# Kernel optimization log

Hardware: AMD Instinct MI355X
Metric: run time of the kernel (lower is better)

The kernel has to match this reference:

```python
import jax, jax.numpy as jnp
import numpy as np

B, H, D, K, V, M = 64, 32, 4096, 128, 128, 4095

def setup_inputs() -> dict:
    key = jax.random.key(0)
    ks = jax.random.split(key, 7)
    return {
        "x": jax.random.normal(ks[0], (B, D), dtype=jnp.float32),
        "prev_K": jax.random.normal(ks[1], (B, M, K), dtype=jnp.float32),
        "prev_V": jax.random.normal(ks[2], (B, M, V), dtype=jnp.float32),
        "Wq": jax.random.normal(ks[3], (H, D, K), dtype=jnp.float32),
        "Wk": jax.random.normal(ks[4], (D, K), dtype=jnp.float32),
        "Wv": jax.random.normal(ks[5], (D, V), dtype=jnp.float32),
        "Wo": jax.random.normal(ks[6], (H, V, D), dtype=jnp.float32),
    }

def reference(x, prev_K, prev_V, Wq, Wk, Wv, Wo):
    # Projections
    q = jnp.einsum('bd,hdk->bhk', x, Wq)            # [b,h,k]
    k_new = jnp.einsum('bd,dk->bk', x, Wk)          # [b,k]
    v_new = jnp.einsum('bd,dv->bv', x, Wv)          # [b,v]
    Kc = jnp.concatenate([prev_K, k_new[:, None, :]], axis=1)  # [b,m+1,k]
    Vc = jnp.concatenate([prev_V, v_new[:, None, :]], axis=1)  # [b,m+1,v]
    # Shared-KV attention (MQA)
    logits = jnp.einsum('bhk,bmk->bhm', q, Kc)
    weights = jax.nn.softmax(logits, axis=-1)
    o = jnp.einsum('bhm,bmv->bhv', weights, Vc)
    y = jnp.einsum('bhv,hvd->bd', o, Wo)
    return (y, Kc, Vc)
```

## Files before the change

kernel.cpp:

```cpp
#include <hip/hip_runtime.h>
#include <stdint.h>

#define B_  64
#define H_  32
#define D_  4096
#define KD  128
#define VD  128
#define M_  4095
#define M1_ 4096
#define NCHUNK 32
#define LOG2E 1.44269504088896f

#define WS_P      0ull
#define WS_Q      4456448ull
#define WS_STATS  4718592ull
#define WS_O      4849664ull
#define WS_OPART  5111808ull

#define WAITVL(n) asm volatile("s_waitcnt vmcnt(" #n ") lgkmcnt(0)" ::: "memory")
#define WAITL()  asm volatile("s_waitcnt lgkmcnt(0)" ::: "memory")
#define BAR()    __builtin_amdgcn_s_barrier()

typedef __attribute__((address_space(3))) char lds_char;
typedef const __attribute__((address_space(1))) char glb_char;

__global__ __launch_bounds__(256) void k_proj_partial(
    const float* __restrict__ x, const float* __restrict__ Wq,
    const float* __restrict__ Wk, const float* __restrict__ Wv,
    float* __restrict__ P) {
  __shared__ float xs[64][260];
  const int dc = blockIdx.x;
  const int hx = blockIdx.y;
  const int t  = threadIdx.x;
  const float* xsrc = x + dc * 256;
  #pragma unroll
  for (int j = 0; j < 16; ++j) {
    int f = t + 256 * j;
    int row = f >> 6, c4 = f & 63;
    *(float4*)&xs[row][c4 * 4] =
        *(const float4*)(xsrc + (size_t)row * D_ + c4 * 4);
  }
  __syncthreads();
  const int bq = t >> 4;
  const int kg = t & 15;
  const int b0 = bq * 4;
  const float* W = (hx < H_) ? (Wq + (size_t)hx * D_ * KD)
                             : ((hx == H_) ? Wk : Wv);
  const float* wp = W + (size_t)(dc * 256) * KD + kg * 8;
  float acc[4][8];
  #pragma unroll
  for (int i = 0; i < 4; ++i)
    #pragma unroll
    for (int j = 0; j < 8; ++j) acc[i][j] = 0.f;
  #pragma unroll 8
  for (int d = 0; d < 256; ++d) {
    float4 w0 = *(const float4*)(wp + (size_t)d * KD);
    float4 w1 = *(const float4*)(wp + (size_t)d * KD + 4);
    float xv[4];
    #pragma unroll
    for (int i = 0; i < 4; ++i) xv[i] = xs[b0 + i][d];
    #pragma unroll
    for (int i = 0; i < 4; ++i) {
      acc[i][0] += xv[i] * w0.x; acc[i][1] += xv[i] * w0.y;
      acc[i][2] += xv[i] * w0.z; acc[i][3] += xv[i] * w0.w;
      acc[i][4] += xv[i] * w1.x; acc[i][5] += xv[i] * w1.y;
      acc[i][6] += xv[i] * w1.z; acc[i][7] += xv[i] * w1.w;
    }
  }
  #pragma unroll
  for (int i = 0; i < 4; ++i) {
    size_t base = ((size_t)(dc * 64 + b0 + i) * 34 + hx) * KD + kg * 8;
    *(float4*)&P[base]     = make_float4(acc[i][0], acc[i][1], acc[i][2], acc[i][3]);
    *(float4*)&P[base + 4] = make_float4(acc[i][4], acc[i][5], acc[i][6], acc[i][7]);
  }
}

__global__ __launch_bounds__(256) void k_proj_reduce(
    const float* __restrict__ P, float* __restrict__ q,
    float* __restrict__ Kc, float* __restrict__ Vc) {
  int i = blockIdx.x * 256 + threadIdx.x;
  int k = i & 127;
  int hx = (i >> 7) % 34;
  int b = i / (128 * 34);
  float s = 0.f;
  #pragma unroll
  for (int dc = 0; dc < 16; ++dc)
    s += P[(size_t)dc * (64 * 34 * 128) + (size_t)(b * 34 + hx) * 128 + k];
  if (hx < H_)       q[((size_t)b * H_ + hx) * KD + k] = s;
  else if (hx == H_) Kc[((size_t)b * M1_ + M_) * KD + k] = s;
  else               Vc[((size_t)b * M1_ + M_) * VD + k] = s;
}

__device__ __forceinline__ void stage_issue(
    const float* src, const float* app_row, float* lbuf, int m_lo, int t) {
  const int wb = t & ~63;
  #pragma unroll
  for (int j = 0; j < 4; ++j) {
    int f = j * 256 + t;
    int r = f >> 5, p = f & 31;
    int m = m_lo + r;
    int g4 = p ^ (r & 7);
    const float* gp = (m < M_) ? (src + (size_t)m * 128 + g4 * 4)
                               : (app_row + g4 * 4);
    __builtin_amdgcn_global_load_lds(
        (glb_char*)gp, (lds_char*)(lbuf + (size_t)(j * 256 + wb) * 4),
        16, 0, 0);
  }
}

__device__ __forceinline__ void copy_out(
    const float* lbuf, float* dst, int m_lo, int t) {
  #pragma unroll
  for (int jj = 0; jj < 4; ++jj) {
    int f = jj * 256 + t;
    int r = f >> 5, p = f & 31;
    int g4 = p ^ (r & 7);
    float4 v = *(const float4*)&lbuf[(size_t)f * 4];
    *(float4*)(dst + (size_t)(m_lo + r) * 128 + g4 * 4) = v;
  }
}

__global__ __launch_bounds__(256, 3) void k_flash(
    const float* __restrict__ prevK, const float* __restrict__ prevV,
    const float* __restrict__ q, float* __restrict__ Kc, float* __restrict__ Vc,
    float* __restrict__ o_part, float* __restrict__ stats) {
  __shared__ float buf[2][32 * 128];
  __shared__ float upool[4608];
  __shared__ float swl[4 * 64];
  const int chunk = blockIdx.x;
  const int b = blockIdx.y;
  const int t = threadIdx.x;
  const int m0 = chunk * 128;
  const int w = t >> 6, l = t & 63;

  const float* kbase = prevK + (size_t)b * M_ * KD;
  const float* vbase = prevV + (size_t)b * M_ * VD;
  const float* kapp  = Kc + ((size_t)b * M1_ + M_) * KD;
  const float* vapp  = Vc + ((size_t)b * M1_ + M_) * VD;
  float* kc = Kc + (size_t)b * M1_ * KD;
  float* vc = Vc + (size_t)b * M1_ * VD;

  float* kslice = &buf[0][0] + w * 2048;
  const int mw = m0 + w * 32;

#define KSTAGE(S)                                                             \
  {                                                                           \
    float* dst_ = kslice + ((S) & 1) * 1024;                                  \
    _Pragma("unroll")                                                         \
    for (int j = 0; j < 4; ++j) {                                             \
      int f4 = j * 64 + l;                                                    \
      int r = f4 >> 5, p = f4 & 31;                                           \
      int m = mw + (S) * 8 + r;                                               \
      int g4 = p ^ r;                                                         \
      const float* gp = (m < M_) ? (kbase + (size_t)m * 128 + g4 * 4)         \
                                 : (kapp + g4 * 4);                           \
      __builtin_amdgcn_global_load_lds(                                       \
          (glb_char*)gp, (lds_char*)(dst_ + j * 256), 16, 0, 0);              \
    }                                                                         \
  }

#define KCOPY(S)                                                              \
  {                                                                           \
    const float* s_ = kslice + ((S) & 1) * 1024;                              \
    _Pragma("unroll")                                                         \
    for (int jj = 0; jj < 4; ++jj) {                                          \
      int f4 = jj * 64 + l;                                                   \
      int r = f4 >> 5, p = f4 & 31;                                           \
      int g4 = p ^ r;                                                         \
      float4 v = *(const float4*)&s_[f4 * 4];                                 \
      *(float4*)(kc + (size_t)(mw + (S) * 8 + r) * 128 + g4 * 4) = v;         \
    }                                                                         \
  }

  const float* qsrc = q + (size_t)b * H_ * KD;
  float4 qv4[4];
  #pragma unroll
  for (int j = 0; j < 4; ++j) {
    int f = j * 256 + t;
    qv4[j] = *(const float4*)(qsrc + (size_t)(f >> 5) * KD + (f & 31) * 4);
  }
  KSTAGE(0); KSTAGE(1);
  #pragma unroll
  for (int j = 0; j < 4; ++j) {
    int f = j * 256 + t;
    int row = f >> 5, c4 = f & 31;
    *(float4*)&upool[row * 128 + ((c4 ^ ((row >> 1) & 7)) * 4)] = qv4[j];
  }

  const int rp = l & 3, hg = l >> 2, h0 = hg * 2;
  const int qsw = hg & 7;
  const int v4 = t & 31, hoct = t >> 5, h0v = hoct * 4;

  float accL0[8], accL1[8];

#define KLOG(S)                                                               \
  {                                                                           \
    const float* lb = kslice + ((S) & 1) * 1024;                              \
    float c00 = 0.f, c01 = 0.f, c10 = 0.f, c11 = 0.f;                         \
    _Pragma("unroll 8")                                                       \
    for (int k4 = 0; k4 < 32; ++k4) {                                         \
      int qp = (k4 ^ qsw) * 4;          \
      float4 qa = *(const float4*)&upool[h0 * 128 + qp];                      \
      float4 qb = *(const float4*)&upool[(h0 + 1) * 128 + qp];                \
      float4 k0v = *(const float4*)&lb[(rp * 32 + (k4 ^ rp)) * 4];            \
      float4 k1v = *(const float4*)&lb[((rp + 4) * 32 + (k4 ^ (rp + 4))) * 4];\
      c00 += qa.x*k0v.x + qa.y*k0v.y + qa.z*k0v.z + qa.w*k0v.w;               \
      c01 += qa.x*k1v.x + qa.y*k1v.y + qa.z*k1v.z + qa.w*k1v.w;               \
      c10 += qb.x*k0v.x + qb.y*k0v.y + qb.z*k0v.z + qb.w*k0v.w;               \
      c11 += qb.x*k1v.x + qb.y*k1v.y + qb.z*k1v.z + qb.w*k1v.w;               \
    }                                                                         \
    accL0[(S)*2] = c00; accL0[(S)*2+1] = c01;                                 \
    accL1[(S)*2] = c10; accL1[(S)*2+1] = c11;                                 \
  }

#define PV_TILE(S, BUFI)                                                      \
  {                                                                           \
    const float* lb = &buf[BUFI][0];                                          \
    _Pragma("unroll 4")                                                       \
    for (int mm = 0; mm < 32; ++mm) {                                         \
      int p = (v4 ^ (mm & 7)) * 4;                                            \
      float4 gv = *(const float4*)&lb[mm * 128 + p];                          \
      float4 w4 = *(const float4*)&upool[((S) * 32 + mm) * 36 + h0v];         \
      a0.x += w4.x*gv.x; a0.y += w4.x*gv.y; a0.z += w4.x*gv.z; a0.w += w4.x*gv.w; \
      a1.x += w4.y*gv.x; a1.y += w4.y*gv.y; a1.z += w4.y*gv.z; a1.w += w4.y*gv.w; \
      a2.x += w4.z*gv.x; a2.y += w4.z*gv.y; a2.z += w4.z*gv.z; a2.w += w4.z*gv.w; \
      a3.x += w4.w*gv.x; a3.y += w4.w*gv.y; a3.z += w4.w*gv.z; a3.w += w4.w*gv.w; \
    }                                                                         \
  }

  WAITL(); BAR();

  WAITVL(4);  KLOG(0); KCOPY(0); KSTAGE(2);
  WAITVL(8);  KLOG(1); KCOPY(1); KSTAGE(3);
  WAITVL(8);  KLOG(2); KCOPY(2);
  WAITVL(4);  KLOG(3); KCOPY(3);

  float mx0 = -3.402823466e38f, mx1 = -3.402823466e38f;
  #pragma unroll
  for (int j = 0; j < 8; ++j) {
    mx0 = fmaxf(mx0, accL0[j]);
    mx1 = fmaxf(mx1, accL1[j]);
  }
  mx0 = fmaxf(mx0, __shfl_xor(mx0, 1)); mx0 = fmaxf(mx0, __shfl_xor(mx0, 2));
  mx1 = fmaxf(mx1, __shfl_xor(mx1, 1)); mx1 = fmaxf(mx1, __shfl_xor(mx1, 2));
  float s0 = 0.f, s1 = 0.f;
  #pragma unroll
  for (int j = 0; j < 8; ++j) {
    float e0 = exp2f((accL0[j] - mx0) * LOG2E); accL0[j] = e0; s0 += e0;
    float e1 = exp2f((accL1[j] - mx1) * LOG2E); accL1[j] = e1; s1 += e1;
  }
  s0 += __shfl_xor(s0, 1); s0 += __shfl_xor(s0, 2);
  s1 += __shfl_xor(s1, 1); s1 += __shfl_xor(s1, 2);
  if (rp == 0)
    *(float4*)&swl[w * 64 + h0 * 2] = make_float4(mx0, s0, mx1, s1);
  WAITL(); BAR();

  stage_issue(vbase, vapp, &buf[0][0], m0, t);
  float cm0, cs0, cm1, cs1;
  {
    float4 r0 = *(const float4*)&swl[0 * 64 + h0 * 2];
    float4 r1 = *(const float4*)&swl[1 * 64 + h0 * 2];
    float4 r2 = *(const float4*)&swl[2 * 64 + h0 * 2];
    float4 r3 = *(const float4*)&swl[3 * 64 + h0 * 2];
    cm0 = fmaxf(fmaxf(r0.x, r1.x), fmaxf(r2.x, r3.x));
    cm1 = fmaxf(fmaxf(r0.z, r1.z), fmaxf(r2.z, r3.z));
    cs0 = r0.y * exp2f((r0.x - cm0) * LOG2E) + r1.y * exp2f((r1.x - cm0) * LOG2E)
        + r2.y * exp2f((r2.x - cm0) * LOG2E) + r3.y * exp2f((r3.x - cm0) * LOG2E);
    cs1 = r0.w * exp2f((r0.z - cm1) * LOG2E) + r1.w * exp2f((r1.z - cm1) * LOG2E)
        + r2.w * exp2f((r2.z - cm1) * LOG2E) + r3.w * exp2f((r3.z - cm1) * LOG2E);
    float f0 = exp2f((mx0 - cm0) * LOG2E);
    float f1 = exp2f((mx1 - cm1) * LOG2E);
    #pragma unroll
    for (int S = 0; S < 4; ++S)
      #pragma unroll
      for (int half = 0; half < 2; ++half) {
        int m = w * 32 + S * 8 + rp + 4 * half;
        upool[m * 36 + h0]     = accL0[S * 2 + half] * f0;
        upool[m * 36 + h0 + 1] = accL1[S * 2 + half] * f1;
      }
  }
  stage_issue(vbase, vapp, &buf[1][0], m0 + 32, t);
  WAITVL(4); BAR();

  float4 a0 = {0,0,0,0}, a1 = {0,0,0,0}, a2 = {0,0,0,0}, a3 = {0,0,0,0};

  PV_TILE(0, 0); copy_out(&buf[0][0], vc, m0, t);
  WAITL(); BAR();
  stage_issue(vbase, vapp, &buf[0][0], m0 + 64, t);
  WAITVL(8); BAR();
  PV_TILE(1, 1); copy_out(&buf[1][0], vc, m0 + 32, t);
  WAITL(); BAR();
  stage_issue(vbase, vapp, &buf[1][0], m0 + 96, t);
  WAITVL(8); BAR();
  PV_TILE(2, 0); copy_out(&buf[0][0], vc, m0 + 64, t);
  WAITVL(4); BAR();
  PV_TILE(3, 1); copy_out(&buf[1][0], vc, m0 + 96, t);

  size_t base = ((size_t)(chunk * B_ + b) * H_ + h0v) * VD + v4 * 4;
  *(float4*)&o_part[base]          = a0;
  *(float4*)&o_part[base + VD]     = a1;
  *(float4*)&o_part[base + 2 * VD] = a2;
  *(float4*)&o_part[base + 3 * VD] = a3;

  if (w == 0 && rp == 0) {
    size_t sb0 = (((size_t)b * H_ + h0) * NCHUNK + chunk) * 2;
    *(float2*)&stats[sb0] = make_float2(cm0, cs0);
    size_t sb1 = (((size_t)b * H_ + h0 + 1) * NCHUNK + chunk) * 2;
    *(float2*)&stats[sb1] = make_float2(cm1, cs1);
  }
#undef KSTAGE
#undef KCOPY
#undef KLOG
#undef PV_TILE
}

__global__ __launch_bounds__(128) void k_combine(
    const float* __restrict__ o_part, const float* __restrict__ stats,
    float* __restrict__ o) {
  const int bh = blockIdx.x;
  const int t = threadIdx.x;
  __shared__ float st[64];
  if (t < 64) st[t] = stats[(size_t)bh * 64 + t];
  __syncthreads();
  float M = -3.402823466e38f;
  #pragma unroll
  for (int c = 0; c < NCHUNK; ++c) M = fmaxf(M, st[2 * c]);
  float wc[NCHUNK];
  float denom = 0.f;
  #pragma unroll
  for (int c = 0; c < NCHUNK; ++c) {
    float e = exp2f((st[2 * c] - M) * LOG2E);
    wc[c] = e;
    denom += st[2 * c + 1] * e;
  }
  const float inv = 1.0f / denom;
  const int b = bh >> 5, h = bh & 31;
  float acc = 0.f;
  #pragma unroll 4
  for (int c = 0; c < NCHUNK; ++c)
    acc += wc[c] * o_part[((size_t)(c * B_ + b) * H_ + h) * VD + t];
  o[(size_t)bh * VD + t] = acc * inv;
}

__global__ __launch_bounds__(256) void k_out_partial(
    const float* __restrict__ o, const float* __restrict__ Wo,
    float* __restrict__ Py) {
  __shared__ float os[64][260];
  const int dc = blockIdx.x;
  const int hvc = blockIdx.y;
  const int t = threadIdx.x;
  #pragma unroll
  for (int j = 0; j < 16; ++j) {
    int f = t + 256 * j;
    int row = f >> 6, c4 = f & 63;
    *(float4*)&os[row][c4 * 4] =
        *(const float4*)(o + (size_t)row * 4096 + hvc * 256 + c4 * 4);
  }
  __syncthreads();
  const int bq = t >> 4, dg = t & 15;
  const int b0 = bq * 4;
  const float* wp = Wo + (size_t)(hvc * 256) * D_ + dc * 128 + dg * 8;
  float acc[4][8];
  #pragma unroll
  for (int i = 0; i < 4; ++i)
    #pragma unroll
    for (int j = 0; j < 8; ++j) acc[i][j] = 0.f;
  #pragma unroll 8
  for (int hv = 0; hv < 256; ++hv) {
    float4 w0 = *(const float4*)(wp + (size_t)hv * D_);
    float4 w1 = *(const float4*)(wp + (size_t)hv * D_ + 4);
    float ov[4];
    #pragma unroll
    for (int i = 0; i < 4; ++i) ov[i] = os[b0 + i][hv];
    #pragma unroll
    for (int i = 0; i < 4; ++i) {
      acc[i][0] += ov[i] * w0.x; acc[i][1] += ov[i] * w0.y;
      acc[i][2] += ov[i] * w0.z; acc[i][3] += ov[i] * w0.w;
      acc[i][4] += ov[i] * w1.x; acc[i][5] += ov[i] * w1.y;
      acc[i][6] += ov[i] * w1.z; acc[i][7] += ov[i] * w1.w;
    }
  }
  #pragma unroll
  for (int i = 0; i < 4; ++i) {
    size_t base = ((size_t)hvc * 64 + b0 + i) * 4096 + dc * 128 + dg * 8;
    *(float4*)&Py[base]     = make_float4(acc[i][0], acc[i][1], acc[i][2], acc[i][3]);
    *(float4*)&Py[base + 4] = make_float4(acc[i][4], acc[i][5], acc[i][6], acc[i][7]);
  }
}

__global__ __launch_bounds__(256) void k_yreduce(
    const float* __restrict__ Py, float* __restrict__ y) {
  int i = blockIdx.x * 256 + threadIdx.x;
  float s = 0.f;
  #pragma unroll
  for (int c = 0; c < 16; ++c) s += Py[(size_t)c * 262144 + i];
  y[i] = s;
}

extern "C" void kernel_launch(void* const* d_in, const int* in_sizes, int n_in,
                              void* d_out, int out_size, void* d_ws, size_t ws_size,
                              hipStream_t stream) {
  const float* x     = (const float*)d_in[0];
  const float* prevK = (const float*)d_in[1];
  const float* prevV = (const float*)d_in[2];
  const float* Wq    = (const float*)d_in[3];
  const float* Wk    = (const float*)d_in[4];
  const float* Wv    = (const float*)d_in[5];
  const float* Wo    = (const float*)d_in[6];

  float* y  = (float*)d_out;
  float* Kc = y + (size_t)B_ * D_;
  float* Vc = Kc + (size_t)B_ * M1_ * KD;

  float* ws     = (float*)d_ws;
  float* P      = ws + WS_P;
  float* q      = ws + WS_Q;
  float* stats  = ws + WS_STATS;
  float* o      = ws + WS_O;
  float* o_part = ws + WS_OPART;

  k_proj_partial<<<dim3(16, 34), 256, 0, stream>>>(x, Wq, Wk, Wv, P);
  k_proj_reduce<<<1088, 256, 0, stream>>>(P, q, Kc, Vc);
  k_flash<<<dim3(32, 64), 256, 0, stream>>>(prevK, prevV, q, Kc, Vc, o_part, stats);
  k_combine<<<2048, 128, 0, stream>>>(o_part, stats, o);
  k_out_partial<<<dim3(32, 16), 256, 0, stream>>>(o, Wo, P);
  k_yreduce<<<1024, 256, 0, stream>>>(P, y);
}
```

Baseline: 267.0 us.

## Split PV stage into per-wave V slices with cross-wave reduction instead of barriers

After: 308.6 us. 15.6% more time.

```diff
diff --git a/kernel.cpp b/kernel.cpp
--- a/kernel.cpp
+++ b/kernel.cpp
@@ -24,6 +24,9 @@
 typedef __attribute__((address_space(3))) char lds_char;
 typedef const __attribute__((address_space(1))) char glb_char;
 
+#define FMA4(A, W, G) { (A).x += (W)*(G).x; (A).y += (W)*(G).y; \
+                        (A).z += (W)*(G).z; (A).w += (W)*(G).w; }
+
 __global__ __launch_bounds__(256) void k_proj_partial(
     const float* __restrict__ x, const float* __restrict__ Wq,
     const float* __restrict__ Wk, const float* __restrict__ Wv,
@@ -89,35 +92,6 @@
   if (hx < H_)       q[((size_t)b * H_ + hx) * KD + k] = s;
   else if (hx == H_) Kc[((size_t)b * M1_ + M_) * KD + k] = s;
   else               Vc[((size_t)b * M1_ + M_) * VD + k] = s;
-}
-
-__device__ __forceinline__ void stage_issue(
-    const float* src, const float* app_row, float* lbuf, int m_lo, int t) {
-  const int wb = t & ~63;
-  #pragma unroll
-  for (int j = 0; j < 4; ++j) {
-    int f = j * 256 + t;
-    int r = f >> 5, p = f & 31;
-    int m = m_lo + r;
-    int g4 = p ^ (r & 7);
-    const float* gp = (m < M_) ? (src + (size_t)m * 128 + g4 * 4)
-                               : (app_row + g4 * 4);
-    __builtin_amdgcn_global_load_lds(
-        (glb_char*)gp, (lds_char*)(lbuf + (size_t)(j * 256 + wb) * 4),
-        16, 0, 0);
-  }
-}
-
-__device__ __forceinline__ void copy_out(
-    const float* lbuf, float* dst, int m_lo, int t) {
-  #pragma unroll
-  for (int jj = 0; jj < 4; ++jj) {
-    int f = jj * 256 + t;
-    int r = f >> 5, p = f & 31;
-    int g4 = p ^ (r & 7);
-    float4 v = *(const float4*)&lbuf[(size_t)f * 4];
-    *(float4*)(dst + (size_t)(m_lo + r) * 128 + g4 * 4) = v;
-  }
 }
 
 __global__ __launch_bounds__(256, 3) void k_flash(
@@ -143,7 +117,7 @@
   float* kslice = &buf[0][0] + w * 2048;
   const int mw = m0 + w * 32;
 
-#define KSTAGE(S)                                                             \
+#define WSTAGE(S, srcb, appr)                                                 \
   {                                                                           \
     float* dst_ = kslice + ((S) & 1) * 1024;                                  \
     _Pragma("unroll")                                                         \
@@ -152,14 +126,14 @@
       int r = f4 >> 5, p = f4 & 31;                                           \
       int m = mw + (S) * 8 + r;                                               \
       int g4 = p ^ r;                                                         \
-      const float* gp = (m < M_) ? (kbase + (size_t)m * 128 + g4 * 4)         \
-                                 : (kapp + g4 * 4);                           \
+      const float* gp = (m < M_) ? ((srcb) + (size_t)m * 128 + g4 * 4)        \
+                                 : ((appr) + g4 * 4);                         \
       __builtin_amdgcn_global_load_lds(                                       \
           (glb_char*)gp, (lds_char*)(dst_ + j * 256), 16, 0, 0);              \
     }                                                                         \
   }
 
-#define KCOPY(S)                                                              \
+#define WCOPY(S, dstp)                                                        \
   {                                                                           \
     const float* s_ = kslice + ((S) & 1) * 1024;                              \
     _Pragma("unroll")                                                         \
@@ -168,7 +142,7 @@
       int r = f4 >> 5, p = f4 & 31;                                           \
       int g4 = p ^ r;                                                         \
       float4 v = *(const float4*)&s_[f4 * 4];                                 \
-      *(float4*)(kc + (size_t)(mw + (S) * 8 + r) * 128 + g4 * 4) = v;         \
+      *(float4*)((dstp) + (size_t)(mw + (S) * 8 + r) * 128 + g4 * 4) = v;     \
     }                                                                         \
   }
 
@@ -179,7 +153,7 @@
     int f = j * 256 + t;
     qv4[j] = *(const float4*)(qsrc + (size_t)(f >> 5) * KD + (f & 31) * 4);
   }
-  KSTAGE(0); KSTAGE(1);
+  WSTAGE(0, kbase, kapp); WSTAGE(1, kbase, kapp);
   #pragma unroll
   for (int j = 0; j < 4; ++j) {
     int f = j * 256 + t;
@@ -189,7 +163,9 @@
 
   const int rp = l & 3, hg = l >> 2, h0 = hg * 2;
   const int qsw = hg & 7;
-  const int v4 = t & 31, hoct = t >> 5, h0v = hoct * 4;
+  const int hi8 = l >> 3, vi8 = l & 7;
+  const int h0v4 = hi8 * 4, vq0 = vi8 * 4;
+  const int wrow0 = w * 32;
 
   float accL0[8], accL1[8];
 
@@ -213,27 +189,35 @@
     accL1[(S)*2] = c10; accL1[(S)*2+1] = c11;                                 \
   }
 
-#define PV_TILE(S, BUFI)                                                      \
+  float4 av[4][4];
+
+#define PV4(S)                                                                \
   {                                                                           \
-    const float* lb = &buf[BUFI][0];                                          \
-    _Pragma("unroll 4")                                                       \
-    for (int mm = 0; mm < 32; ++mm) {                                         \
-      int p = (v4 ^ (mm & 7)) * 4;                                            \
-      float4 gv = *(const float4*)&lb[mm * 128 + p];                          \
-      float4 w4 = *(const float4*)&upool[((S) * 32 + mm) * 36 + h0v];         \
-      a0.x += w4.x*gv.x; a0.y += w4.x*gv.y; a0.z += w4.x*gv.z; a0.w += w4.x*gv.w; \
-      a1.x += w4.y*gv.x; a1.y += w4.y*gv.y; a1.z += w4.y*gv.z; a1.w += w4.y*gv.w; \
-      a2.x += w4.z*gv.x; a2.y += w4.z*gv.y; a2.z += w4.z*gv.z; a2.w += w4.z*gv.w; \
-      a3.x += w4.w*gv.x; a3.y += w4.w*gv.y; a3.z += w4.w*gv.z; a3.w += w4.w*gv.w; \
+    const float* lb = kslice + ((S) & 1) * 1024;                              \
+    _Pragma("unroll")                                                         \
+    for (int mm = 0; mm < 8; ++mm) {                                          \
+      float4 w4 = *(const float4*)&upool[(wrow0 + (S) * 8 + mm) * 36 + h0v4]; \
+      float4 g0 = *(const float4*)&lb[(mm * 32 + ((vq0 + 0) ^ mm)) * 4];      \
+      float4 g1 = *(const float4*)&lb[(mm * 32 + ((vq0 + 1) ^ mm)) * 4];      \
+      float4 g2 = *(const float4*)&lb[(mm * 32 + ((vq0 + 2) ^ mm)) * 4];      \
+      float4 g3 = *(const float4*)&lb[(mm * 32 + ((vq0 + 3) ^ mm)) * 4];      \
+      FMA4(av[0][0], w4.x, g0); FMA4(av[0][1], w4.x, g1);                     \
+      FMA4(av[0][2], w4.x, g2); FMA4(av[0][3], w4.x, g3);                     \
+      FMA4(av[1][0], w4.y, g0); FMA4(av[1][1], w4.y, g1);                     \
+      FMA4(av[1][2], w4.y, g2); FMA4(av[1][3], w4.y, g3);                     \
+      FMA4(av[2][0], w4.z, g0); FMA4(av[2][1], w4.z, g1);                     \
+      FMA4(av[2][2], w4.z, g2); FMA4(av[2][3], w4.z, g3);                     \
+      FMA4(av[3][0], w4.w, g0); FMA4(av[3][1], w4.w, g1);                     \
+      FMA4(av[3][2], w4.w, g2); FMA4(av[3][3], w4.w, g3);                     \
     }                                                                         \
   }
 
   WAITL(); BAR();
 
-  WAITVL(4);  KLOG(0); KCOPY(0); KSTAGE(2);
-  WAITVL(8);  KLOG(1); KCOPY(1); KSTAGE(3);
-  WAITVL(8);  KLOG(2); KCOPY(2);
-  WAITVL(4);  KLOG(3); KCOPY(3);
+  WAITVL(4);  KLOG(0); WCOPY(0, kc); WSTAGE(2, kbase, kapp);
+  WAITVL(8);  KLOG(1); WCOPY(1, kc); WSTAGE(3, kbase, kapp);
+  WAITVL(8);  KLOG(2); WCOPY(2, kc);
+  WAITVL(4);  KLOG(3); WCOPY(3, kc);
 
   float mx0 = -3.402823466e38f, mx1 = -3.402823466e38f;
   #pragma unroll
@@ -255,7 +239,7 @@
     *(float4*)&swl[w * 64 + h0 * 2] = make_float4(mx0, s0, mx1, s1);
   WAITL(); BAR();
 
-  stage_issue(vbase, vapp, &buf[0][0], m0, t);
+  WSTAGE(0, vbase, vapp);
   float cm0, cs0, cm1, cs1;
   {
     float4 r0 = *(const float4*)&swl[0 * 64 + h0 * 2];
@@ -274,33 +258,58 @@
     for (int S = 0; S < 4; ++S)
       #pragma unroll
       for (int half = 0; half < 2; ++half) {
-        int m = w * 32 + S * 8 + rp + 4 * half;
+        int m = wrow0 + S * 8 + rp + 4 * half;
         upool[m * 36 + h0]     = accL0[S * 2 + half] * f0;
         upool[m * 36 + h0 + 1] = accL1[S * 2 + half] * f1;
       }
   }
-  stage_issue(vbase, vapp, &buf[1][0], m0 + 32, t);
-  WAITVL(4); BAR();
-
-  float4 a0 = {0,0,0,0}, a1 = {0,0,0,0}, a2 = {0,0,0,0}, a3 = {0,0,0,0};
-
-  PV_TILE(0, 0); copy_out(&buf[0][0], vc, m0, t);
+  WSTAGE(1, vbase, vapp);
+
+  #pragma unroll
+  for (int hh = 0; hh < 4; ++hh)
+    #pragma unroll
+    for (int k = 0; k < 4; ++k) av[hh][k] = make_float4(0.f, 0.f, 0.f, 0.f);
+
+  WAITVL(4);  PV4(0); WCOPY(0, vc); WSTAGE(2, vbase, vapp);
+  WAITVL(8);  PV4(1); WCOPY(1, vc); WSTAGE(3, vbase, vapp);
+  WAITVL(8);  PV4(2); WCOPY(2, vc);
+  WAITVL(4);  PV4(3); WCOPY(3, vc);
+
+  float* red = &buf[0][0];
+  BAR();
+  if ((w & 1) == 0) {
+    float* r_ = red + (w >> 1) * 4096;
+    #pragma unroll
+    for (int i = 0; i < 16; ++i)
+      *(float4*)&r_[(l * 16 + (i ^ (l & 15))) * 4] = av[i >> 2][i & 3];
+  }
   WAITL(); BAR();
-  stage_issue(vbase, vapp, &buf[0][0], m0 + 64, t);
-  WAITVL(8); BAR();
-  PV_TILE(1, 1); copy_out(&buf[1][0], vc, m0 + 32, t);
+  if (w & 1) {
+    const float* r_ = red + (w >> 1) * 4096;
+    #pragma unroll
+    for (int i = 0; i < 16; ++i) {
+      float4 p = *(const float4*)&r_[(l * 16 + (i ^ (l & 15))) * 4];
+      av[i >> 2][i & 3].x += p.x; av[i >> 2][i & 3].y += p.y;
+      av[i >> 2][i & 3].z += p.z; av[i >> 2][i & 3].w += p.w;
+    }
+  }
+  if (w == 1) {
+    #pragma unroll
+    for (int i = 0; i < 16; ++i)
+      *(float4*)&red[(l * 16 + (i ^ (l & 15))) * 4] = av[i >> 2][i & 3];
+  }
   WAITL(); BAR();
-  stage_issue(vbase, vapp, &buf[1][0], m0 + 96, t);
-  WAITVL(8); BAR();
-  PV_TILE(2, 0); copy_out(&buf[0][0], vc, m0 + 64, t);
-  WAITVL(4); BAR();
-  PV_TILE(3, 1); copy_out(&buf[1][0], vc, m0 + 96, t);
-
-  size_t base = ((size_t)(chunk * B_ + b) * H_ + h0v) * VD + v4 * 4;
-  *(float4*)&o_part[base]          = a0;
-  *(float4*)&o_part[base + VD]     = a1;
-  *(float4*)&o_part[base + 2 * VD] = a2;
-  *(float4*)&o_part[base + 3 * VD] = a3;
+  if (w == 3) {
+    size_t obase = ((size_t)(chunk * B_ + b) * H_) * VD;
+    #pragma unroll
+    for (int i = 0; i < 16; ++i) {
+      float4 p = *(const float4*)&red[(l * 16 + (i ^ (l & 15))) * 4];
+      int hh = i >> 2, k = i & 3;
+      float4 s = av[hh][k];
+      s.x += p.x; s.y += p.y; s.z += p.z; s.w += p.w;
+      *(float4*)&o_part[obase + (size_t)(h0v4 + hh) * VD + vq0 * 4 + k * 4] = s;
+    }
+  }
 
   if (w == 0 && rp == 0) {
     size_t sb0 = (((size_t)b * H_ + h0) * NCHUNK + chunk) * 2;
@@ -308,10 +317,10 @@
     size_t sb1 = (((size_t)b * H_ + h0 + 1) * NCHUNK + chunk) * 2;
     *(float2*)&stats[sb1] = make_float2(cm1, cs1);
   }
-#undef KSTAGE
-#undef KCOPY
+#undef WSTAGE
+#undef WCOPY
 #undef KLOG
-#undef PV_TILE
+#undef PV4
 }
 
 __global__ __launch_bounds__(128) void k_combine(
```
